# Kernel tuning notes

Measured on AMD Instinct MI355X. Metric: run time of the kernel, lower is better.

## Reference

```python
import jax, jax.numpy as jnp
import numpy as np

COMMITMENT_COST = 0.25


def setup_inputs() -> dict:
    key = jax.random.key(0)
    k1, k2 = jax.random.split(key)
    inputs = jax.random.normal(k1, (64, 4096, 64), dtype=jnp.float32)
    codewords = jax.random.normal(k2, (512, 64), dtype=jnp.float32)
    return {"inputs": inputs, "codewords": codewords}


def reference(inputs, codewords):
    D = codewords.shape[-1]
    flat = inputs.reshape(-1, D)  # (N, D)
    # squared Euclidean distances (N, K) via expansion, avoiding the (N, K, D) tensor
    x_sq = jnp.sum(flat * flat, axis=-1, keepdims=True)          # (N, 1)
    c_sq = jnp.sum(codewords * codewords, axis=-1)               # (K,)
    distances = x_sq - 2.0 * (flat @ codewords.T) + c_sq         # (N, K)
    encoding_indices = jnp.argmin(distances, axis=1)             # (N,)
    quantized = jnp.take(codewords, encoding_indices, axis=0).reshape(inputs.shape)
    commitment_loss = jnp.mean((jax.lax.stop_gradient(quantized) - inputs) ** 2)
    loss = COMMITMENT_COST * commitment_loss
    encoding_indices = encoding_indices.reshape(inputs.shape[:-1])
    return quantized, encoding_indices, loss
```

## Files before the change

kernel.cpp:

```cpp
#include <hip/hip_runtime.h>


typedef _Float16 half8 __attribute__((ext_vector_type(8)));
typedef float    floatx4 __attribute__((ext_vector_type(4)));

#define NVEC  262144
#define DDIM  64
#define KCW   512
#define LOSS_SCALE (0.25f / 16777216.0f)
#define DMARGIN 0.005f
#define BROWS 128
#define NBLK  (NVEC / BROWS)
#define CHUNK 64

#define WS_CSQ   0
#define WS_CSQH  2048
#define WS_HL    8192

__global__ void prep_kernel(const float* __restrict__ cw,
                            float* __restrict__ csq,
                            float* __restrict__ csqh,
                            _Float16* __restrict__ cw_hl,
                            float* __restrict__ loss_slot) {
    int n = blockIdx.x * blockDim.x + threadIdx.x;
    if (n < KCW) {
        const float4* r = (const float4*)(cw + n * DDIM);
        _Float16* orow = cw_hl + n * 128;
        float s = 0.f;
        #pragma unroll
        for (int t = 0; t < 8; ++t) {
            float4 a = r[2 * t], b = r[2 * t + 1];
            half8 hh, ll;
            #pragma unroll
            for (int i = 0; i < 4; ++i) {
                float v = ((const float*)&a)[i];
                s += v * v;
                _Float16 h = (_Float16)v;
                hh[i] = h; ll[i] = (_Float16)(v - (float)h);
                v = ((const float*)&b)[i];
                s += v * v;
                h = (_Float16)v;
                hh[4 + i] = h; ll[4 + i] = (_Float16)(v - (float)h);
            }
            *(half8*)(orow + 8 * t) = hh;
            *(half8*)(orow + 64 + 8 * t) = ll;
        }
        csq[n]  = s;
        csqh[n] = 0.5f * s;
    }
    if (n == 0) *loss_slot = 0.f;
}

__global__ void vq_mfma_kernel(const float* __restrict__ x,
                               const float* __restrict__ cw,
                               const _Float16* __restrict__ cw_hl,
                               const float* __restrict__ csqh,
                               const float* __restrict__ csq,
                               float* __restrict__ out_q,
                               float* __restrict__ out_idx,
                               float* __restrict__ out_loss) {
    __shared__ _Float16      Bs[CHUNK * 136];
    __shared__ float         csqhs[KCW];
    __shared__ int           win[BROWS];
    __shared__ int           lslist[BROWS];
    __shared__ unsigned char flg[BROWS];
    __shared__ float         red[4];
    __shared__ unsigned      lcnt;

    const int tid  = threadIdx.x;
    const int w    = tid >> 6;
    const int lane = tid & 63;
    const int quad = lane >> 4;
    const int col  = lane & 15;
    const int blk  = blockIdx.x * BROWS;

    if (tid == 0) lcnt = 0u;
    csqhs[tid]       = -csqh[tid];
    csqhs[tid + 256] = -csqh[tid + 256];

    half8 ah0[2], ah1[2], al0[2], al1[2];
    #pragma unroll
    for (int rt = 0; rt < 2; ++rt) {
        const float* xr = x + (size_t)(blk + w * 32 + rt * 16 + col) * DDIM;
        float4 f0 = *(const float4*)(xr + quad * 8);
        float4 f1 = *(const float4*)(xr + quad * 8 + 4);
        float4 g0 = *(const float4*)(xr + 32 + quad * 8);
        float4 g1 = *(const float4*)(xr + 32 + quad * 8 + 4);
        #pragma unroll
        for (int i = 0; i < 4; ++i) {
            float v = ((const float*)&f0)[i];
            _Float16 h = (_Float16)v;
            ah0[rt][i] = h; al0[rt][i] = (_Float16)(v - (float)h);
            v = ((const float*)&f1)[i]; h = (_Float16)v;
            ah0[rt][4 + i] = h; al0[rt][4 + i] = (_Float16)(v - (float)h);
            v = ((const float*)&g0)[i]; h = (_Float16)v;
            ah1[rt][i] = h; al1[rt][i] = (_Float16)(v - (float)h);
            v = ((const float*)&g1)[i]; h = (_Float16)v;
            ah1[rt][4 + i] = h; al1[rt][4 + i] = (_Float16)(v - (float)h);
        }
    }

    float M1[8], M2[8];
    int   idx[8];
    #pragma unroll
    for (int s = 0; s < 8; ++s) {
        M1[s] = -3.402823466e38f; M2[s] = -3.402823466e38f; idx[s] = 0;
    }

    for (int ch = 0; ch < 8; ++ch) {
        __syncthreads();
        {
            const int nl  = tid >> 2;
            const int seg = tid & 3;
            const half8* src =
                (const half8*)(cw_hl + (((size_t)(ch * CHUNK + nl)) << 7) + seg * 32);
            half8* dst = (half8*)(Bs + nl * 136 + seg * 32);
            #pragma unroll
            for (int b = 0; b < 4; ++b) dst[b] = src[b];
        }
        __syncthreads();

        #pragma unroll 2
        for (int t = 0; t < 4; ++t) {
            const int n  = ch * CHUNK + t * 16 + col;
            const int nb = (t * 16 + col) * 136;
            half8 bh0 = *(const half8*)&Bs[nb + quad * 8];
            half8 bh1 = *(const half8*)&Bs[nb + 32 + quad * 8];
            half8 bl0 = *(const half8*)&Bs[nb + 64 + quad * 8];
            half8 bl1 = *(const half8*)&Bs[nb + 96 + quad * 8];
            const float vn = csqhs[n];

            #pragma unroll
            for (int rt = 0; rt < 2; ++rt) {
                floatx4 acc = {vn, vn, vn, vn};
                acc = __builtin_amdgcn_mfma_f32_16x16x32_f16(ah0[rt], bh0, acc, 0, 0, 0);
                acc = __builtin_amdgcn_mfma_f32_16x16x32_f16(ah1[rt], bh1, acc, 0, 0, 0);
                acc = __builtin_amdgcn_mfma_f32_16x16x32_f16(al0[rt], bh0, acc, 0, 0, 0);
                acc = __builtin_amdgcn_mfma_f32_16x16x32_f16(al1[rt], bh1, acc, 0, 0, 0);
                acc = __builtin_amdgcn_mfma_f32_16x16x32_f16(ah0[rt], bl0, acc, 0, 0, 0);
                acc = __builtin_amdgcn_mfma_f32_16x16x32_f16(ah1[rt], bl1, acc, 0, 0, 0);
                #pragma unroll
                for (int reg = 0; reg < 4; ++reg) {
                    int s = rt * 4 + reg;
                    float d = acc[reg];
                    if (d > M1[s]) idx[s] = n;
                    M2[s] = __builtin_amdgcn_fmed3f(M1[s], M2[s], d);
                    M1[s] = fmaxf(M1[s], d);
                }
            }
        }
    }

    #pragma unroll
    for (int off = 1; off < 16; off <<= 1) {
        #pragma unroll
        for (int s = 0; s < 8; ++s) {
            float o1 = __shfl_xor(M1[s], off, 16);
            float o2 = __shfl_xor(M2[s], off, 16);
            int   oi = __shfl_xor(idx[s], off, 16);
            float mn = fminf(M1[s], o1);
            M2[s] = fmaxf(fmaxf(M2[s], o2), mn);
            if (o1 > M1[s] || (o1 == M1[s] && oi < idx[s])) idx[s] = oi;
            M1[s] = fmaxf(M1[s], o1);
        }
    }

    if (col < 4) {
        #pragma unroll
        for (int rt = 0; rt < 2; ++rt) {
            int s  = rt * 4 + col;
            int rl = w * 32 + rt * 16 + quad * 4 + col;
            int nw = idx[s];
            int f  = (M1[s] - M2[s] <= DMARGIN) ? 1 : 0;
            win[rl] = nw;
            flg[rl] = (unsigned char)f;
            out_idx[blk + rl] = (float)nw;
            if (f) { unsigned p = atomicAdd(&lcnt, 1u); lslist[p] = rl; }
        }
    }
    __syncthreads();

    float ls = 0.f;
    #pragma unroll
    for (int k = 0; k < 8; ++k) {
        int rl = k * 16 + (tid >> 4);
        int e4 = (tid & 15) * 4;
        int wn = win[rl];
        int f  = flg[rl];
        float4 q  = *(const float4*)(cw + wn * DDIM + e4);
        float4 xv = *(const float4*)(x + (size_t)(blk + rl) * DDIM + e4);
        *(float4*)(out_q + (size_t)(blk + rl) * DDIM + e4) = q;
        if (!f) {
            float d0 = q.x - xv.x, d1 = q.y - xv.y;
            float d2 = q.z - xv.z, d3 = q.w - xv.w;
            ls += d0 * d0 + d1 * d1 + d2 * d2 + d3 * d3;
        }
    }
    #pragma unroll
    for (int off = 32; off > 0; off >>= 1) ls += __shfl_down(ls, off, 64);
    if (lane == 0) red[w] = ls;
    __syncthreads();
    if (tid == 0)
        atomicAdd(out_loss, ((red[0] + red[1]) + (red[2] + red[3])) * LOSS_SCALE);

    const unsigned cnt = lcnt;
    const int grp = tid >> 4;
    const int tx  = tid & 15;
    for (unsigned i = (unsigned)grp; i < cnt; i += 16) {
        const int rl = lslist[i];
        const size_t row = (size_t)blk + rl;

        float4 xr[16];
        const float4* xg = (const float4*)(x + row * DDIM);
        #pragma unroll
        for (int t = 0; t < 16; ++t) xr[t] = xg[t];

        float best = 3.402823466e38f; int bi = 0;
        for (int j = 0; j < 32; ++j) {
            int n = tx + 16 * j;
            const float4* c = (const float4*)(cw + n * DDIM);
            float a0 = 0.f, a1 = 0.f, a2 = 0.f, a3 = 0.f;
            #pragma unroll
            for (int t = 0; t < 16; ++t) {
                float4 cv = c[t];
                a0 = __builtin_fmaf(xr[t].x, cv.x, a0);
                a1 = __builtin_fmaf(xr[t].y, cv.y, a1);
                a2 = __builtin_fmaf(xr[t].z, cv.z, a2);
                a3 = __builtin_fmaf(xr[t].w, cv.w, a3);
            }
            float sc = __builtin_fmaf(-2.f, (a0 + a1) + (a2 + a3), csq[n]);
            if (sc < best) { best = sc; bi = n; }
        }
        #pragma unroll
        for (int off = 8; off > 0; off >>= 1) {
            float d2 = __shfl_down(best, off, 16);
            int   i2 = __shfl_down(bi,   off, 16);
            if (d2 < best || (d2 == best && i2 < bi)) { best = d2; bi = i2; }
        }
        if (tx == 0) {
            out_idx[row] = (float)bi;
            const float4* qg = (const float4*)(cw + bi * DDIM);
            float4* og = (float4*)(out_q + row * DDIM);
            float lf = 0.f;
            #pragma unroll
            for (int t = 0; t < 16; ++t) {
                float4 q = qg[t];
                og[t] = q;
                float d0 = q.x - xr[t].x, d1 = q.y - xr[t].y;
                float d2_ = q.z - xr[t].z, d3 = q.w - xr[t].w;
                lf += d0 * d0 + d1 * d1 + d2_ * d2_ + d3 * d3;
            }
            atomicAdd(out_loss, lf * LOSS_SCALE);
        }
    }
}

extern "C" void kernel_launch(void* const* d_in, const int* in_sizes, int n_in,
                              void* d_out, int out_size, void* d_ws, size_t ws_size,
                              hipStream_t stream) {
    const float* x  = (const float*)d_in[0];
    const float* cw = (const float*)d_in[1];
    float* out      = (float*)d_out;
    float* out_q    = out;
    float* out_idx  = out + 16777216;
    float* out_loss = out + 16777216 + 262144;

    char* ws = (char*)d_ws;
    float*    csq   = (float*)(ws + WS_CSQ);
    float*    csqh  = (float*)(ws + WS_CSQH);
    _Float16* cw_hl = (_Float16*)(ws + WS_HL);

    prep_kernel<<<2, 256, 0, stream>>>(cw, csq, csqh, cw_hl, out_loss);
    vq_mfma_kernel<<<NBLK, 256, 0, stream>>>(x, cw, cw_hl, csqh, csq,
                                             out_q, out_idx, out_loss);
}
```

Before: 217.0 us.

## Double-buffer codeword chunks via direct global-to-LDS loads with XOR swizzle

Codeword staging into shared memory now uses two LDS buffers. The next chunk is prefetched with global_load_lds (when that builtin exists) while the current chunk feeds the MFMAs, which removes one barrier per chunk and overlaps load latency with compute. The prep kernel stores each codeword row in an XOR-swizzled 16-byte-segment layout, replacing the padded 136-stride layout to avoid LDS bank conflicts without padding. The cost is double the LDS footprint, which may reduce occupancy. Correctness relies on the swizzle matching between the prep kernel and the reads.

New measurement: 218.8 us. About the same (+0.8%).

```diff
diff --git a/kernel.cpp b/kernel.cpp
--- a/kernel.cpp
+++ b/kernel.cpp
@@ -12,6 +12,12 @@
 #define BROWS 128
 #define NBLK  (NVEC / BROWS)
 #define CHUNK 64
+
+#if defined(__has_builtin)
+#if __has_builtin(__builtin_amdgcn_global_load_lds)
+#define HAS_GLL 1
+#endif
+#endif
 
 #define WS_CSQ   0
 #define WS_CSQH  2048
@@ -26,6 +32,7 @@
     if (n < KCW) {
         const float4* r = (const float4*)(cw + n * DDIM);
         _Float16* orow = cw_hl + n * 128;
+        const int kx = n & 7;
         float s = 0.f;
         #pragma unroll
         for (int t = 0; t < 8; ++t) {
@@ -42,8 +49,8 @@
                 h = (_Float16)v;
                 hh[4 + i] = h; ll[4 + i] = (_Float16)(v - (float)h);
             }
-            *(half8*)(orow + 8 * t) = hh;
-            *(half8*)(orow + 64 + 8 * t) = ll;
+            *(half8*)(orow + ((t ^ kx) << 3))       = hh;
+            *(half8*)(orow + (((8 + t) ^ kx) << 3)) = ll;
         }
         csq[n]  = s;
         csqh[n] = 0.5f * s;
@@ -59,7 +66,7 @@
                                float* __restrict__ out_q,
                                float* __restrict__ out_idx,
                                float* __restrict__ out_loss) {
-    __shared__ _Float16      Bs[CHUNK * 136];
+    __shared__ __align__(16) _Float16 Bs[2 * CHUNK * 128];
     __shared__ float         csqhs[KCW];
     __shared__ int           win[BROWS];
     __shared__ int           lslist[BROWS];
@@ -73,6 +80,7 @@
     const int quad = lane >> 4;
     const int col  = lane & 15;
     const int blk  = blockIdx.x * BROWS;
+    char* BsB = (char*)Bs;
 
     if (tid == 0) lcnt = 0u;
     csqhs[tid]       = -csqh[tid];
@@ -107,27 +115,43 @@
         M1[s] = -3.402823466e38f; M2[s] = -3.402823466e38f; idx[s] = 0;
     }
 
+    auto STAGE = [&](int b, int ch) {
+#ifdef HAS_GLL
+        const char* g = (const char*)cw_hl + (ch << 14) + (w << 12) + (lane << 4);
+        const char* l = BsB + (b << 14) + (w << 12);
+        #pragma unroll
+        for (int k = 0; k < 4; ++k) {
+            __builtin_amdgcn_global_load_lds(
+                (const __attribute__((address_space(1))) void*)(g + (k << 10)),
+                (__attribute__((address_space(3))) void*)(l + (k << 10)),
+                16, 0, 0);
+        }
+#else
+        const char* g = (const char*)cw_hl + (ch << 14) + (w << 12) + (lane << 4);
+        char* l = BsB + (b << 14) + (w << 12) + (lane << 4);
+        #pragma unroll
+        for (int k = 0; k < 4; ++k)
+            *(half8*)(l + (k << 10)) = *(const half8*)(g + (k << 10));
+#endif
+    };
+
+    STAGE(0, 0);
+    const int kx = col & 7;
+    int cur = 0;
+    #pragma unroll 1
     for (int ch = 0; ch < 8; ++ch) {
+        asm volatile("s_waitcnt vmcnt(0)" ::: "memory");
         __syncthreads();
-        {
-            const int nl  = tid >> 2;
-            const int seg = tid & 3;
-            const half8* src =
-                (const half8*)(cw_hl + (((size_t)(ch * CHUNK + nl)) << 7) + seg * 32);
-            half8* dst = (half8*)(Bs + nl * 136 + seg * 32);
-            #pragma unroll
-            for (int b = 0; b < 4; ++b) dst[b] = src[b];
-        }
-        __syncthreads();
+        if (ch < 7) STAGE(cur ^ 1, ch + 1);
 
         #pragma unroll 2
         for (int t = 0; t < 4; ++t) {
-            const int n  = ch * CHUNK + t * 16 + col;
-            const int nb = (t * 16 + col) * 136;
-            half8 bh0 = *(const half8*)&Bs[nb + quad * 8];
-            half8 bh1 = *(const half8*)&Bs[nb + 32 + quad * 8];
-            half8 bl0 = *(const half8*)&Bs[nb + 64 + quad * 8];
-            half8 bl1 = *(const half8*)&Bs[nb + 96 + quad * 8];
+            const int n    = ch * CHUNK + t * 16 + col;
+            const char* rb = BsB + (cur << 14) + ((t * 16 + col) << 8);
+            half8 bh0 = *(const half8*)(rb + (((quad)      ^ kx) << 4));
+            half8 bh1 = *(const half8*)(rb + (((4  + quad) ^ kx) << 4));
+            half8 bl0 = *(const half8*)(rb + (((8  + quad) ^ kx) << 4));
+            half8 bl1 = *(const half8*)(rb + (((12 + quad) ^ kx) << 4));
             const float vn = csqhs[n];
 
             #pragma unroll
@@ -149,6 +173,7 @@
                 }
             }
         }
+        cur ^= 1;
     }
 
     #pragma unroll
```
